# Optimization experiments

Measured on AMD Instinct MI355X. Metric: run time of the kernel, lower is better.

The kernel has to match this reference:

```python
import jax, jax.numpy as jnp
import numpy as np

B, N, DIM = 8, 8192, 256
K, CDIM = 4096, 1024
COMMIT = 0.25


def setup_inputs() -> dict:
    key = jax.random.key(0)
    ks = jax.random.split(key, 4)
    x = jax.random.normal(ks[0], (B, N, DIM), dtype=jnp.float32)
    ln_g = jnp.ones((DIM,), jnp.float32)
    ln_b = jnp.zeros((DIM,), jnp.float32)
    w_pre = jax.random.normal(ks[1], (DIM, CDIM), jnp.float32) / np.sqrt(DIM)
    b_pre = jnp.zeros((CDIM,), jnp.float32)
    embed = jax.random.normal(ks[2], (K, CDIM), jnp.float32)
    w_post = jax.random.normal(ks[3], (CDIM, DIM), jnp.float32) / np.sqrt(CDIM)
    b_post = jnp.zeros((DIM,), jnp.float32)
    return {"x": x, "ln_g": ln_g, "ln_b": ln_b, "w_pre": w_pre, "b_pre": b_pre,
            "embed": embed, "w_post": w_post, "b_post": b_post}


def reference(x, ln_g, ln_b, w_pre, b_pre, embed, w_post, b_post):
    # LayerNorm over last dim (eps=1e-5, torch default)
    mu = jnp.mean(x, axis=-1, keepdims=True)
    var = jnp.mean((x - mu) ** 2, axis=-1, keepdims=True)
    xn = (x - mu) * jax.lax.rsqrt(var + 1e-5) * ln_g + ln_b
    # GELU (exact, erf-based as in torch default) then Linear dim->codebook_dim
    z_e = jax.nn.gelu(xn, approximate=False) @ w_pre + b_pre  # (B,N,CDIM)
    flat = z_e.reshape(-1, CDIM)                              # (B*N, CDIM)
    # squared euclidean distances to codebook, argmin, gather
    z_sq = jnp.sum(flat * flat, axis=1, keepdims=True)        # (BN,1)
    e_sq = jnp.sum(embed * embed, axis=1)                     # (K,)
    dist = z_sq - 2.0 * (flat @ embed.T) + e_sq[None, :]      # (BN,K)
    indices = jnp.argmin(dist, axis=1)                        # (BN,)
    z_q = embed[indices]                                      # (BN,CDIM)
    # commitment loss (z_q detached)
    commit = COMMIT * jnp.mean((flat - jax.lax.stop_gradient(z_q)) ** 2)
    # straight-through estimator
    z_q_st = flat + jax.lax.stop_gradient(z_q - flat)
    z_q_st = z_q_st.reshape(B, N, CDIM)
    quantized = z_q_st @ w_post + b_post                      # (B,N,DIM)
    return quantized, indices.reshape(B, N), commit
```

## Files before the change

### kernel.cpp

```cpp
#include <hip/hip_runtime.h>

#define BN_ROWS 65536
#define DIMX 256
#define CDIM 1024
#define KCODES 4096
#define NSP 16
#define CMARG 2.5f
#define RMARG 1.2f
#define FLT_BIG 3.402823466e+38f

static const size_t OFF_ESQ   = 0;
static const size_t OFF_IDXF  = 16384;
static const size_t OFF_CROW  = 278528;
static const size_t OFF_EPOST = 540672;
static const size_t OFF_EH    = 4734976;
static const size_t OFF_NFLAG = 13123584;
static const size_t OFF_FLAG  = 13123648;
static const size_t OFF_CAND  = 13385792;

typedef __attribute__((ext_vector_type(8))) short bf16x8;
typedef __attribute__((ext_vector_type(4))) float f32x4;

#define GLOAD_LDS16(gsrc, ldst)                                                \
  __builtin_amdgcn_global_load_lds(                                            \
      (const __attribute__((address_space(1))) void*)(gsrc),                   \
      (__attribute__((address_space(3))) void*)(ldst), 16, 0, 0)

template <int VMC>
__device__ __forceinline__ void wait_vm() {
  if constexpr (VMC == 8)
    asm volatile("s_waitcnt vmcnt(8)" ::: "memory");
  else if constexpr (VMC == 4)
    asm volatile("s_waitcnt vmcnt(4)" ::: "memory");
  else
    asm volatile("s_waitcnt vmcnt(0)" ::: "memory");
}

__device__ inline unsigned short bf_rtn(float f) {
  unsigned u = __float_as_uint(f);
  unsigned r = (u + 0x7FFFu + ((u >> 16) & 1u)) >> 16;
  return (unsigned short)r;
}
__device__ inline unsigned fkey(float s) {
  unsigned b = __float_as_uint(s);
  return b ^ ((unsigned)((int)b >> 31) | 0x80000000u);
}
__device__ inline float keyinv(unsigned k) {
  unsigned b = (k & 0x80000000u) ? (k ^ 0x80000000u) : ~k;
  return __uint_as_float(b);
}

__global__ __launch_bounds__(256) void k_esq(const float* __restrict__ embed,
                                             float* __restrict__ e_sq) {
  const int t = threadIdx.x, wv = t >> 6, lane = t & 63;
  const int row = blockIdx.x * 4 + wv;
  const float* e = embed + (size_t)row * CDIM;
  float s = 0.f;
  for (int k = lane * 4; k < CDIM; k += 256) {
    float4 v = *(const float4*)(e + k);
    s = fmaf(v.x, v.x, s); s = fmaf(v.y, v.y, s);
    s = fmaf(v.z, v.z, s); s = fmaf(v.w, v.w, s);
  }
#pragma unroll
  for (int o = 32; o > 0; o >>= 1) s += __shfl_xor(s, o);
  if (lane == 0) e_sq[row] = s;
}

__global__ __launch_bounds__(256) void k_ehi(const float* __restrict__ embed,
                                             short* __restrict__ Eh) {
  const int t = threadIdx.x;
  const size_t row = blockIdx.x;
  float4 v = *(const float4*)(embed + row * CDIM + t * 4);
  *(short4*)(Eh + row * CDIM + t * 4) =
      make_short4((short)bf_rtn(v.x), (short)bf_rtn(v.y), (short)bf_rtn(v.z),
                  (short)bf_rtn(v.w));
}

__global__ __launch_bounds__(256) void k_ln_gelu_gemm(
    const float* __restrict__ x, const float* __restrict__ ln_g,
    const float* __restrict__ ln_b, const float* __restrict__ w_pre,
    const float* __restrict__ b_pre, float* __restrict__ zf,
    short* __restrict__ zh, int row0) {
  __shared__ float g[16][DIMX];
  const int t = threadIdx.x;
  const int lrow0 = blockIdx.x * 16;
  const int grow0 = row0 + lrow0;
  const int wv = t >> 6, lane = t & 63;
#pragma unroll
  for (int j = 0; j < 4; ++j) {
    const int r = wv * 4 + j;
    const float* xr = x + (size_t)(grow0 + r) * DIMX;
    float4 v = *(const float4*)(xr + lane * 4);
    float s = v.x + v.y + v.z + v.w;
    float ss = v.x * v.x + v.y * v.y + v.z * v.z + v.w * v.w;
#pragma unroll
    for (int o = 32; o > 0; o >>= 1) { s += __shfl_xor(s, o); ss += __shfl_xor(ss, o); }
    const float mu = s * (1.0f / 256.0f);
    const float var = ss * (1.0f / 256.0f) - mu * mu;
    const float rstd = rsqrtf(var + 1e-5f);
    float vv[4] = {v.x, v.y, v.z, v.w};
#pragma unroll
    for (int q = 0; q < 4; ++q) {
      const int d = lane * 4 + q;
      float xn = (vv[q] - mu) * rstd * ln_g[d] + ln_b[d];
      g[r][d] = 0.5f * xn * (1.0f + erff(xn * 0.70710678118654752f));
    }
  }
  __syncthreads();
  float acc[16][4];
#pragma unroll
  for (int r = 0; r < 16; ++r)
#pragma unroll
    for (int c = 0; c < 4; ++c) acc[r][c] = 0.f;
#pragma unroll 4
  for (int d = 0; d < DIMX; ++d) {
    float4 w = *(const float4*)(w_pre + (size_t)d * CDIM + t * 4);
#pragma unroll
    for (int r = 0; r < 16; ++r) {
      const float gv = g[r][d];
      acc[r][0] = fmaf(gv, w.x, acc[r][0]);
      acc[r][1] = fmaf(gv, w.y, acc[r][1]);
      acc[r][2] = fmaf(gv, w.z, acc[r][2]);
      acc[r][3] = fmaf(gv, w.w, acc[r][3]);
    }
  }
  float4 bp = *(const float4*)(b_pre + t * 4);
#pragma unroll
  for (int r = 0; r < 16; ++r) {
    float4 o;
    o.x = acc[r][0] + bp.x; o.y = acc[r][1] + bp.y;
    o.z = acc[r][2] + bp.z; o.w = acc[r][3] + bp.w;
    *(float4*)(zf + (size_t)(lrow0 + r) * CDIM + t * 4) = o;
    *(short4*)(zh + (size_t)(lrow0 + r) * CDIM + t * 4) =
        make_short4((short)bf_rtn(o.x), (short)bf_rtn(o.y), (short)bf_rtn(o.z),
                    (short)bf_rtn(o.w));
  }
}

__global__ __launch_bounds__(512) void k_score(
    const short* __restrict__ Eh, const short* __restrict__ Zh,
    const float* __restrict__ e_sq, uint2* __restrict__ cand, int chunk) {
  __shared__ __align__(16) short lds[4][16384];
  const int t = threadIdx.x;
  const int cpx = gridDim.x >> 3;
  const int bx = (blockIdx.x & 7) * cpx + (blockIdx.x >> 3);
  const int zblk = bx / NSP, csp = bx % NSP;
  const int wid = t >> 6, l = t & 63;
  const int wr = wid >> 2, wc = wid & 3;
  const int lg = l >> 4, lo16 = l & 15;
  const int rowbase = zblk * 256;
  const int m0 = csp * 256;
  const int wr8 = wr * 8, wc4 = wc * 4, l8 = l * 8;

  const bool isA = (wid < 4);
  const int q = wid & 3;
  const short* sarr = isA ? Eh : Zh;
  const int sbase = isA ? m0 : rowbase;
  const short* sp0 = sarr + (size_t)(sbase + q * 64 + lo16) * 1024 + lg * 8;
  const int dstbase = (isA ? 0 : 8192) + q * 4 * 512;

  f32x4 acc[8][4];
#pragma unroll
  for (int mi = 0; mi < 8; ++mi)
#pragma unroll
    for (int ni = 0; ni < 4; ++ni) acc[mi][ni] = (f32x4){0.f, 0.f, 0.f, 0.f};

#pragma unroll
  for (int pk = 0; pk < 3; ++pk) {
    const short* sp = sp0 + pk * 32;
    short* D = &lds[pk][dstbase];
#pragma unroll
    for (int u = 0; u < 4; ++u) GLOAD_LDS16(sp + u * 16384, D + u * 512);
  }

#define SCORE_KT(KT, VMC, ST)                                                  \
  {                                                                            \
    const short* Lc = lds[(KT) & 3];                                           \
    wait_vm<VMC>();                                                            \
    __builtin_amdgcn_s_barrier();                                              \
    __builtin_amdgcn_sched_barrier(0);                                         \
    bf16x8 bh[4], a[8];                                                        \
    _Pragma("unroll") for (int ni = 0; ni < 4; ++ni) bh[ni] =                  \
        *(const bf16x8*)(Lc + 8192 + (wc4 + ni) * 512 + l8);                   \
    _Pragma("unroll") for (int u = 0; u < 8; ++u) a[u] =                       \
        *(const bf16x8*)(Lc + (wr8 + u) * 512 + l8);                           \
    if (ST) {                                                                  \
      short* Dst = &lds[((KT) + 3) & 3][dstbase];                              \
      const short* spk = sp0 + ((KT) + 3) * 32;                                \
      _Pragma("unroll") for (int u = 0; u < 4; ++u)                            \
          GLOAD_LDS16(spk + u * 16384, Dst + u * 512);                         \
    }                                                                          \
    asm volatile("s_waitcnt lgkmcnt(0)" ::: "memory");                         \
    __builtin_amdgcn_sched_barrier(0);                                         \
    __builtin_amdgcn_s_setprio(1);                                             \
    _Pragma("unroll") for (int u = 0; u < 8; ++u)                              \
        _Pragma("unroll") for (int ni = 0; ni < 4; ++ni) acc[u][ni] =          \
            __builtin_amdgcn_mfma_f32_16x16x32_bf16(a[u], bh[ni],              \
                                                    acc[u][ni], 0, 0, 0);      \
    __builtin_amdgcn_s_setprio(0);                                             \
  }

  for (int kt = 0; kt < 30; ++kt) SCORE_KT(kt, 8, (kt < 29));
  SCORE_KT(30, 4, false);
  SCORE_KT(31, 0, false);
#undef SCORE_KT

  float s1[4];
  int i1[4];
#pragma unroll
  for (int i = 0; i < 4; ++i) { s1[i] = FLT_BIG; i1[i] = 0x7fffffff; }
#pragma unroll
  for (int mi = 0; mi < 8; ++mi) {
    const int c0 = m0 + wr * 128 + mi * 16 + lg * 4;
    float4 es = *(const float4*)(e_sq + c0);
    float esv[4] = {es.x, es.y, es.z, es.w};
#pragma unroll
    for (int ni = 0; ni < 4; ++ni) {
#pragma unroll
      for (int j = 0; j < 4; ++j) {
        const float s = fmaf(-2.0f, acc[mi][ni][j], esv[j]);
        const int c = c0 + j;
        if (s < s1[ni] || (s == s1[ni] && c < i1[ni])) { s1[ni] = s; i1[ni] = c; }
      }
    }
  }

  unsigned long long* red = (unsigned long long*)&lds[0][0];
  float* sb = (float*)&lds[0][2048];
  unsigned* sbi = (unsigned*)&lds[0][2560];
  unsigned* cnt = (unsigned*)&lds[0][3072];
  uint2* slot = (uint2*)&lds[0][3584];

  __syncthreads();
#pragma unroll
  for (int ni = 0; ni < 4; ++ni) {
    unsigned long long k1v =
        (((unsigned long long)fkey(s1[ni])) << 32) | (unsigned)i1[ni];
    unsigned long long o1 = __shfl_xor(k1v, 16);
    k1v = o1 < k1v ? o1 : k1v;
    o1 = __shfl_xor(k1v, 32);
    k1v = o1 < k1v ? o1 : k1v;
    if (lg == 0) {
      const int r = wc * 64 + ni * 16 + lo16;
      red[r * 2 + wr] = k1v;
    }
  }
  __syncthreads();
  if (t < 256) {
    unsigned long long a1 = red[t * 2 + 0], b1 = red[t * 2 + 1];
    if (b1 < a1) a1 = b1;
    sb[t] = keyinv((unsigned)(a1 >> 32));
    sbi[t] = (unsigned)(a1 & 0xFFFFFFFFull);
    cnt[t] = 0;
  }
  __syncthreads();
#pragma unroll
  for (int mi = 0; mi < 8; ++mi) {
    const int c0 = m0 + wr * 128 + mi * 16 + lg * 4;
    float4 es = *(const float4*)(e_sq + c0);
    float esv[4] = {es.x, es.y, es.z, es.w};
#pragma unroll
    for (int ni = 0; ni < 4; ++ni) {
      const int r = wc * 64 + ni * 16 + lo16;
      const float thr = sb[r] + CMARG;
#pragma unroll
      for (int j = 0; j < 4; ++j) {
        const float s = fmaf(-2.0f, acc[mi][ni][j], esv[j]);
        const unsigned c = (unsigned)(c0 + j);
        if (s < thr && c != sbi[r]) {
          unsigned pos = atomicAdd(&cnt[r], 1u);
          if (pos < 3) slot[r * 3 + pos] = make_uint2(__float_as_uint(s), c);
        }
      }
    }
  }
  __syncthreads();
  if (t < 256) {
    uint2* g = cand + ((size_t)(rowbase + t) * NSP + csp) * 4;
    const unsigned ov = (cnt[t] > 3) ? 0x40000000u : 0u;
    g[0] = make_uint2(__float_as_uint(sb[t]), sbi[t] | ov);
    const unsigned n = cnt[t] > 3 ? 3 : cnt[t];
#pragma unroll
    for (int k = 0; k < 3; ++k)
      g[1 + k] = (k < (int)n) ? slot[t * 3 + k]
                              : make_uint2(__float_as_uint(FLT_BIG), 0xFFFFFFFFu);
  }
}

__global__ __launch_bounds__(256) void k_refine(
    const uint2* __restrict__ cand, const float* __restrict__ zf,
    const float* __restrict__ embed, int* __restrict__ idxf,
    float* __restrict__ crow, float* __restrict__ out_idx,
    int* __restrict__ flag_rows, int* __restrict__ nflag, int chunk,
    int row0) {
  const int t = threadIdx.x, wid = t >> 6, l = t & 63;
  const int lrow = blockIdx.x * 4 + wid;
  if (lrow >= chunk) return;
  const int grow = row0 + lrow;
  const uint2 cs = cand[(size_t)lrow * 64 + l];
  const float sc = __uint_as_float(cs.x);
  const unsigned raw = cs.y;
  const bool isMin = (l & 3) == 0;
  float gm = isMin ? sc : FLT_BIG;
#pragma unroll
  for (int o = 32; o > 0; o >>= 1) gm = fminf(gm, __shfl_xor(gm, o));
  const float thr = gm + RMARG;
  const bool ovf = __any(isMin && (raw & 0x40000000u) && (sc < thr));

  float zv[16];
#pragma unroll
  for (int j = 0; j < 16; ++j) zv[j] = zf[(size_t)lrow * CDIM + l + 64 * j];

  const int myidx = (int)(raw & 0xFFFFu);
  const bool valid = (sc < thr) && (myidx < KCODES);
  unsigned long long mask = __ballot(valid);
  double d1 = 1e300;
  int i1 = 0x7fffffff;
  while (mask) {
    const int src = __ffsll((unsigned long long)mask) - 1;
    mask &= mask - 1;
    const int c = __shfl(myidx, src);
    const float* e = embed + (size_t)c * CDIM;
    double dd = 0.0;
#pragma unroll
    for (int j = 0; j < 16; ++j) {
      const double df = (double)zv[j] - (double)e[l + 64 * j];
      dd = fma(df, df, dd);
    }
#pragma unroll
    for (int o = 32; o > 0; o >>= 1) dd += __shfl_xor(dd, o);
    if (dd < d1 || (dd == d1 && c < i1)) { d1 = dd; i1 = c; }
  }
  if (l == 0) {
    idxf[grow] = i1;
    out_idx[grow] = (float)i1;
    crow[grow] = (float)d1;
    if (ovf) {
      const int s = atomicAdd(nflag, 1);
      flag_rows[s] = lrow;
    }
  }
}

__global__ __launch_bounds__(256) void k_exact(
    const float* __restrict__ zf, const float* __restrict__ embed,
    const int* __restrict__ flag_rows, const int* __restrict__ nflag,
    int* __restrict__ idxf, float* __restrict__ crow,
    float* __restrict__ out_idx, int row0) {
  __shared__ double wd[4];
  __shared__ int wcidx[4];
  const int t = threadIdx.x;
  const int wid = t >> 6, l = t & 63;
  const int n = *nflag;

  for (int fi = blockIdx.x; fi < n; fi += gridDim.x) {
    const int lrow = flag_rows[fi];
    const int grow = row0 + lrow;
    float zr[16];
#pragma unroll
    for (int j = 0; j < 16; ++j) zr[j] = zf[(size_t)lrow * CDIM + l + 64 * j];
    double dmin = 1e300;
    int cmin = 0x7fffffff;
    for (int ci = 0; ci < 1024; ++ci) {
      const int c = wid * 1024 + ci;
      const float* e = embed + (size_t)c * CDIM;
      double dd = 0.0;
#pragma unroll
      for (int j = 0; j < 16; ++j) {
        const double df = (double)zr[j] - (double)e[l + 64 * j];
        dd = fma(df, df, dd);
      }
#pragma unroll
      for (int o = 32; o > 0; o >>= 1) dd += __shfl_xor(dd, o);
      if (dd < dmin) { dmin = dd; cmin = c; }
    }
    if (l == 0) { wd[wid] = dmin; wcidx[wid] = cmin; }
    __syncthreads();
    if (t == 0) {
      double dm = wd[0]; int cm = wcidx[0];
#pragma unroll
      for (int wv = 1; wv < 4; ++wv) {
        if (wd[wv] < dm || (wd[wv] == dm && wcidx[wv] < cm)) {
          dm = wd[wv]; cm = wcidx[wv];
        }
      }
      idxf[grow] = cm;
      out_idx[grow] = (float)cm;
      crow[grow] = (float)dm;
    }
    __syncthreads();
  }
}

__global__ __launch_bounds__(256) void k_epost(const float* __restrict__ E,
                                               const float* __restrict__ w_post,
                                               float* __restrict__ E_post) {
  __shared__ float es[16][128];
  const int t = threadIdx.x;
  const int r0 = blockIdx.x * 16;
  float acc[16];
#pragma unroll
  for (int r = 0; r < 16; ++r) acc[r] = 0.f;
  for (int k0 = 0; k0 < CDIM; k0 += 128) {
    __syncthreads();
#pragma unroll
    for (int p = 0; p < 2; ++p) {
      const int fl = (p * 256 + t) * 4;
      const int r = fl >> 7, kk = fl & 127;
      float4 v = *(const float4*)(E + (size_t)(r0 + r) * CDIM + k0 + kk);
      *(float4*)&es[r][kk] = v;
    }
    __syncthreads();
#pragma unroll 4
    for (int d = 0; d < 128; ++d) {
      const float w = w_post[(size_t)(k0 + d) * DIMX + t];
#pragma unroll
      for (int r = 0; r < 16; ++r) acc[r] = fmaf(es[r][d], w, acc[r]);
    }
  }
#pragma unroll
  for (int r = 0; r < 16; ++r)
    E_post[(size_t)(r0 + r) * DIMX + t] = acc[r];
}

__global__ __launch_bounds__(256) void k_gather(const float* __restrict__ E_post,
                                                const int* __restrict__ idx,
                                                const float* __restrict__ b_post,
                                                float* __restrict__ outq) {
  const int t = threadIdx.x;
  const int r0 = blockIdx.x * 16;
  const float bp = b_post[t];
#pragma unroll
  for (int i = 0; i < 16; ++i) {
    const int row = r0 + i;
    outq[(size_t)row * DIMX + t] = E_post[(size_t)idx[row] * DIMX + t] + bp;
  }
}

__global__ __launch_bounds__(256) void k_commit_final(
    const float* __restrict__ crow, float* __restrict__ out_commit) {
  const int t = threadIdx.x;
  double s = 0.0;
  for (int i = t; i < BN_ROWS; i += 256) s += (double)crow[i];
#pragma unroll
  for (int o = 32; o > 0; o >>= 1) s += __shfl_xor(s, o);
  __shared__ double wsum[4];
  if ((t & 63) == 0) wsum[t >> 6] = s;
  __syncthreads();
  if (t == 0)
    *out_commit = (float)(0.25 * (wsum[0] + wsum[1] + wsum[2] + wsum[3]) /
                          (65536.0 * 1024.0));
}

extern "C" void kernel_launch(void* const* d_in, const int* in_sizes, int n_in,
                              void* d_out, int out_size, void* d_ws,
                              size_t ws_size, hipStream_t stream) {
  const float* x = (const float*)d_in[0];
  const float* ln_g = (const float*)d_in[1];
  const float* ln_b = (const float*)d_in[2];
  const float* w_pre = (const float*)d_in[3];
  const float* b_pre = (const float*)d_in[4];
  const float* embed = (const float*)d_in[5];
  const float* w_post = (const float*)d_in[6];
  const float* b_post = (const float*)d_in[7];

  float* out = (float*)d_out;
  float* outq = out;
  float* out_idx = out + 16777216;
  float* out_commit = out + 16842752;

  char* ws = (char*)d_ws;
  float* e_sq = (float*)(ws + OFF_ESQ);
  int* idxf = (int*)(ws + OFF_IDXF);
  float* crow = (float*)(ws + OFF_CROW);
  float* E_post = (float*)(ws + OFF_EPOST);
  short* Eh = (short*)(ws + OFF_EH);
  int* nflag = (int*)(ws + OFF_NFLAG);
  int* flag_rows = (int*)(ws + OFF_FLAG);

  int chunk = 4096;
  while (chunk < BN_ROWS &&
         OFF_CAND + (size_t)(chunk * 2) * 6656ull <= ws_size)
    chunk *= 2;
  uint2* cand = (uint2*)(ws + OFF_CAND);
  short* zh = (short*)(ws + OFF_CAND + (size_t)chunk * 512);
  float* zf = (float*)(ws + OFF_CAND + (size_t)chunk * 512 + (size_t)chunk * 2048);

  k_esq<<<KCODES / 4, 256, 0, stream>>>(embed, e_sq);
  k_ehi<<<KCODES, 256, 0, stream>>>(embed, Eh);
  k_epost<<<KCODES / 16, 256, 0, stream>>>(embed, w_post, E_post);

  for (int row0 = 0; row0 < BN_ROWS; row0 += chunk) {
    hipMemsetAsync(nflag, 0, sizeof(int), stream);
    k_ln_gelu_gemm<<<chunk / 16, 256, 0, stream>>>(x, ln_g, ln_b, w_pre, b_pre,
                                                   zf, zh, row0);
    k_score<<<(chunk / 256) * NSP, 512, 0, stream>>>(Eh, zh, e_sq, cand, chunk);
    k_refine<<<chunk / 4, 256, 0, stream>>>(cand, zf, embed, idxf, crow,
                                            out_idx, flag_rows, nflag, chunk,
                                            row0);
    k_exact<<<128, 256, 0, stream>>>(zf, embed, flag_rows, nflag, idxf, crow,
                                     out_idx, row0);
  }

  k_gather<<<BN_ROWS / 16, 256, 0, stream>>>(E_post, idxf, b_post, outq);
  k_commit_final<<<1, 256, 0, stream>>>(crow, out_commit);
}
```

Measured before the change: 1.456 ms.

## Switch codebook scoring GEMM from bf16 to int8 MFMA with wider candidate margins

Quantizes the codebook and z_e to int8 with a fixed scale and runs the distance-scoring GEMM with i32 16x16x64 int8 MFMA instead of bf16. This halves operand bytes and K-loop iterations in the score kernel. Because int8 is coarser, the candidate margin and slot count per split grow (11 slots, margins of 24), so the refine kernel checks more candidates in fp64. The trade is more refine work and wider candidate storage, plus overflow-flag fallbacks if the fixed scale clips values.

```diff
diff --git a/kernel.cpp b/kernel.cpp
--- a/kernel.cpp
+++ b/kernel.cpp
@@ -5,21 +5,24 @@
 #define CDIM 1024
 #define KCODES 4096
 #define NSP 16
-#define CMARG 2.5f
-#define RMARG 1.2f
+#define NSLOT 11
+#define NENT 12
+#define CMARG 24.0f
+#define RMARG 24.0f
+#define QS 24.0f
+#define INV_S2 (1.0f / (QS * QS))
 #define FLT_BIG 3.402823466e+38f
 
 static const size_t OFF_ESQ   = 0;
 static const size_t OFF_IDXF  = 16384;
 static const size_t OFF_CROW  = 278528;
 static const size_t OFF_EPOST = 540672;
-static const size_t OFF_EH    = 4734976;
-static const size_t OFF_NFLAG = 13123584;
-static const size_t OFF_FLAG  = 13123648;
-static const size_t OFF_CAND  = 13385792;
-
-typedef __attribute__((ext_vector_type(8))) short bf16x8;
-typedef __attribute__((ext_vector_type(4))) float f32x4;
+static const size_t OFF_EI8   = 4734976;
+static const size_t OFF_NFLAG = 8929280;
+static const size_t OFF_FLAG  = 8929344;
+static const size_t OFF_CAND  = 9191488;
+
+typedef __attribute__((ext_vector_type(4))) int i32x4;
 
 #define GLOAD_LDS16(gsrc, ldst)                                                \
   __builtin_amdgcn_global_load_lds(                                            \
@@ -36,10 +39,8 @@
     asm volatile("s_waitcnt vmcnt(0)" ::: "memory");
 }
 
-__device__ inline unsigned short bf_rtn(float f) {
-  unsigned u = __float_as_uint(f);
-  unsigned r = (u + 0x7FFFu + ((u >> 16) & 1u)) >> 16;
-  return (unsigned short)r;
+__device__ inline char q8(float f) {
+  return (char)__float2int_rn(fminf(fmaxf(f * QS, -127.f), 127.f));
 }
 __device__ inline unsigned fkey(float s) {
   unsigned b = __float_as_uint(s);
@@ -66,21 +67,20 @@
   if (lane == 0) e_sq[row] = s;
 }
 
-__global__ __launch_bounds__(256) void k_ehi(const float* __restrict__ embed,
-                                             short* __restrict__ Eh) {
+__global__ __launch_bounds__(256) void k_ei8(const float* __restrict__ embed,
+                                             char* __restrict__ Ei8) {
   const int t = threadIdx.x;
   const size_t row = blockIdx.x;
   float4 v = *(const float4*)(embed + row * CDIM + t * 4);
-  *(short4*)(Eh + row * CDIM + t * 4) =
-      make_short4((short)bf_rtn(v.x), (short)bf_rtn(v.y), (short)bf_rtn(v.z),
-                  (short)bf_rtn(v.w));
+  *(char4*)(Ei8 + row * CDIM + t * 4) =
+      make_char4(q8(v.x), q8(v.y), q8(v.z), q8(v.w));
 }
 
 __global__ __launch_bounds__(256) void k_ln_gelu_gemm(
     const float* __restrict__ x, const float* __restrict__ ln_g,
     const float* __restrict__ ln_b, const float* __restrict__ w_pre,
     const float* __restrict__ b_pre, float* __restrict__ zf,
-    short* __restrict__ zh, int row0) {
+    char* __restrict__ zi8, int row0) {
   __shared__ float g[16][DIMX];
   const int t = threadIdx.x;
   const int lrow0 = blockIdx.x * 16;
@@ -131,16 +131,15 @@
     o.x = acc[r][0] + bp.x; o.y = acc[r][1] + bp.y;
     o.z = acc[r][2] + bp.z; o.w = acc[r][3] + bp.w;
     *(float4*)(zf + (size_t)(lrow0 + r) * CDIM + t * 4) = o;
-    *(short4*)(zh + (size_t)(lrow0 + r) * CDIM + t * 4) =
-        make_short4((short)bf_rtn(o.x), (short)bf_rtn(o.y), (short)bf_rtn(o.z),
-                    (short)bf_rtn(o.w));
+    *(char4*)(zi8 + (size_t)(lrow0 + r) * CDIM + t * 4) =
+        make_char4(q8(o.x), q8(o.y), q8(o.z), q8(o.w));
   }
 }
 
 __global__ __launch_bounds__(512) void k_score(
-    const short* __restrict__ Eh, const short* __restrict__ Zh,
+    const char* __restrict__ Ei8, const char* __restrict__ Zi8,
     const float* __restrict__ e_sq, uint2* __restrict__ cand, int chunk) {
-  __shared__ __align__(16) short lds[4][16384];
+  __shared__ __align__(16) char lds[4][32768];
   const int t = threadIdx.x;
   const int cpx = gridDim.x >> 3;
   const int bx = (blockIdx.x & 7) * cpx + (blockIdx.x >> 3);
@@ -150,59 +149,59 @@
   const int lg = l >> 4, lo16 = l & 15;
   const int rowbase = zblk * 256;
   const int m0 = csp * 256;
-  const int wr8 = wr * 8, wc4 = wc * 4, l8 = l * 8;
+  const int wr8 = wr * 8, wc4 = wc * 4, l16 = l * 16;
 
   const bool isA = (wid < 4);
   const int q = wid & 3;
-  const short* sarr = isA ? Eh : Zh;
+  const char* sarr = isA ? Ei8 : Zi8;
   const int sbase = isA ? m0 : rowbase;
-  const short* sp0 = sarr + (size_t)(sbase + q * 64 + lo16) * 1024 + lg * 8;
-  const int dstbase = (isA ? 0 : 8192) + q * 4 * 512;
-
-  f32x4 acc[8][4];
+  const char* sp0 = sarr + (size_t)(sbase + q * 64 + lo16) * 1024 + lg * 16;
+  const int dstbase = (isA ? 0 : 16384) + q * 4096;
+
+  i32x4 acc[8][4];
 #pragma unroll
   for (int mi = 0; mi < 8; ++mi)
 #pragma unroll
-    for (int ni = 0; ni < 4; ++ni) acc[mi][ni] = (f32x4){0.f, 0.f, 0.f, 0.f};
+    for (int ni = 0; ni < 4; ++ni) acc[mi][ni] = (i32x4){0, 0, 0, 0};
 
 #pragma unroll
   for (int pk = 0; pk < 3; ++pk) {
-    const short* sp = sp0 + pk * 32;
-    short* D = &lds[pk][dstbase];
-#pragma unroll
-    for (int u = 0; u < 4; ++u) GLOAD_LDS16(sp + u * 16384, D + u * 512);
+    const char* sp = sp0 + pk * 64;
+    char* D = &lds[pk][dstbase];
+#pragma unroll
+    for (int u = 0; u < 4; ++u) GLOAD_LDS16(sp + u * 16384, D + u * 1024);
   }
 
 #define SCORE_KT(KT, VMC, ST)                                                  \
   {                                                                            \
-    const short* Lc = lds[(KT) & 3];                                           \
+    const char* Lc = lds[(KT) & 3];                                            \
     wait_vm<VMC>();                                                            \
     __builtin_amdgcn_s_barrier();                                              \
     __builtin_amdgcn_sched_barrier(0);                                         \
-    bf16x8 bh[4], a[8];                                                        \
+    i32x4 bh[4], a[8];                                                         \
     _Pragma("unroll") for (int ni = 0; ni < 4; ++ni) bh[ni] =                  \
-        *(const bf16x8*)(Lc + 8192 + (wc4 + ni) * 512 + l8);                   \
+        *(const i32x4*)(Lc + 16384 + (wc4 + ni) * 1024 + l16);                 \
     _Pragma("unroll") for (int u = 0; u < 8; ++u) a[u] =                       \
-        *(const bf16x8*)(Lc + (wr8 + u) * 512 + l8);                           \
+        *(const i32x4*)(Lc + (wr8 + u) * 1024 + l16);                          \
     if (ST) {                                                                  \
-      short* Dst = &lds[((KT) + 3) & 3][dstbase];                              \
-      const short* spk = sp0 + ((KT) + 3) * 32;                                \
+      char* Dst = &lds[((KT) + 3) & 3][dstbase];                               \
+      const char* spk = sp0 + ((KT) + 3) * 64;                                 \
       _Pragma("unroll") for (int u = 0; u < 4; ++u)                            \
-          GLOAD_LDS16(spk + u * 16384, Dst + u * 512);                         \
+          GLOAD_LDS16(spk + u * 16384, Dst + u * 1024);                        \
     }                                                                          \
     asm volatile("s_waitcnt lgkmcnt(0)" ::: "memory");                         \
     __builtin_amdgcn_sched_barrier(0);                                         \
     __builtin_amdgcn_s_setprio(1);                                             \
     _Pragma("unroll") for (int u = 0; u < 8; ++u)                              \
         _Pragma("unroll") for (int ni = 0; ni < 4; ++ni) acc[u][ni] =          \
-            __builtin_amdgcn_mfma_f32_16x16x32_bf16(a[u], bh[ni],              \
-                                                    acc[u][ni], 0, 0, 0);      \
+            __builtin_amdgcn_mfma_i32_16x16x64_i8(a[u], bh[ni],                \
+                                                  acc[u][ni], 0, 0, 0);        \
     __builtin_amdgcn_s_setprio(0);                                             \
   }
 
-  for (int kt = 0; kt < 30; ++kt) SCORE_KT(kt, 8, (kt < 29));
-  SCORE_KT(30, 4, false);
-  SCORE_KT(31, 0, false);
+  for (int kt = 0; kt < 14; ++kt) SCORE_KT(kt, 8, (kt < 13));
+  SCORE_KT(14, 4, false);
+  SCORE_KT(15, 0, false);
 #undef SCORE_KT
 
   float s1[4];
@@ -218,7 +217,7 @@
     for (int ni = 0; ni < 4; ++ni) {
 #pragma unroll
       for (int j = 0; j < 4; ++j) {
-        const float s = fmaf(-2.0f, acc[mi][ni][j], esv[j]);
+        const float s = fmaf(-2.0f * INV_S2, (float)acc[mi][ni][j], esv[j]);
         const int c = c0 + j;
         if (s < s1[ni] || (s == s1[ni] && c < i1[ni])) { s1[ni] = s; i1[ni] = c; }
       }
@@ -226,10 +225,10 @@
   }
 
   unsigned long long* red = (unsigned long long*)&lds[0][0];
-  float* sb = (float*)&lds[0][2048];
-  unsigned* sbi = (unsigned*)&lds[0][2560];
-  unsigned* cnt = (unsigned*)&lds[0][3072];
-  uint2* slot = (uint2*)&lds[0][3584];
+  float* sb = (float*)&lds[0][4096];
+  unsigned* sbi = (unsigned*)&lds[0][5120];
+  unsigned* cnt = (unsigned*)&lds[0][6144];
+  uint2* slot = (uint2*)&lds[0][7168];
 
   __syncthreads();
 #pragma unroll
@@ -265,24 +264,25 @@
       const float thr = sb[r] + CMARG;
 #pragma unroll
       for (int j = 0; j < 4; ++j) {
-        const float s = fmaf(-2.0f, acc[mi][ni][j], esv[j]);
+        const float s = fmaf(-2.0f * INV_S2, (float)acc[mi][ni][j], esv[j]);
         const unsigned c = (unsigned)(c0 + j);
         if (s < thr && c != sbi[r]) {
           unsigned pos = atomicAdd(&cnt[r], 1u);
-          if (pos < 3) slot[r * 3 + pos] = make_uint2(__float_as_uint(s), c);
+          if (pos < NSLOT)
+            slot[r * NSLOT + pos] = make_uint2(__float_as_uint(s), c);
         }
       }
     }
   }
   __syncthreads();
   if (t < 256) {
-    uint2* g = cand + ((size_t)(rowbase + t) * NSP + csp) * 4;
-    const unsigned ov = (cnt[t] > 3) ? 0x40000000u : 0u;
+    uint2* g = cand + (size_t)(rowbase + t) * (NSP * NENT) + csp * NENT;
+    const unsigned ov = (cnt[t] > NSLOT) ? 0x40000000u : 0u;
     g[0] = make_uint2(__float_as_uint(sb[t]), sbi[t] | ov);
-    const unsigned n = cnt[t] > 3 ? 3 : cnt[t];
-#pragma unroll
-    for (int k = 0; k < 3; ++k)
-      g[1 + k] = (k < (int)n) ? slot[t * 3 + k]
+    const unsigned n = cnt[t] > NSLOT ? NSLOT : cnt[t];
+#pragma unroll
+    for (int k = 0; k < NSLOT; ++k)
+      g[1 + k] = (k < (int)n) ? slot[t * NSLOT + k]
                               : make_uint2(__float_as_uint(FLT_BIG), 0xFFFFFFFFu);
   }
 }
@@ -297,40 +297,55 @@
   const int lrow = blockIdx.x * 4 + wid;
   if (lrow >= chunk) return;
   const int grow = row0 + lrow;
-  const uint2 cs = cand[(size_t)lrow * 64 + l];
-  const float sc = __uint_as_float(cs.x);
-  const unsigned raw = cs.y;
-  const bool isMin = (l & 3) == 0;
-  float gm = isMin ? sc : FLT_BIG;
+  const uint2* base = cand + (size_t)lrow * (NSP * NENT);
+  const uint2 e0 = base[l];
+  const uint2 e1 = base[64 + l];
+  const uint2 e2 = base[128 + l];
+  const bool is0 = (l % NENT) == 0;
+  const bool is1 = ((l + 64) % NENT) == 0;
+  const bool is2 = ((l + 128) % NENT) == 0;
+  float gm = FLT_BIG;
+  if (is0) gm = fminf(gm, __uint_as_float(e0.x));
+  if (is1) gm = fminf(gm, __uint_as_float(e1.x));
+  if (is2) gm = fminf(gm, __uint_as_float(e2.x));
 #pragma unroll
   for (int o = 32; o > 0; o >>= 1) gm = fminf(gm, __shfl_xor(gm, o));
   const float thr = gm + RMARG;
-  const bool ovf = __any(isMin && (raw & 0x40000000u) && (sc < thr));
+  bool myovf = (is0 && (e0.y & 0x40000000u) && __uint_as_float(e0.x) < thr) ||
+               (is1 && (e1.y & 0x40000000u) && __uint_as_float(e1.x) < thr) ||
+               (is2 && (e2.y & 0x40000000u) && __uint_as_float(e2.x) < thr);
+  const bool ovf = __any(myovf);
 
   float zv[16];
 #pragma unroll
   for (int j = 0; j < 16; ++j) zv[j] = zf[(size_t)lrow * CDIM + l + 64 * j];
 
-  const int myidx = (int)(raw & 0xFFFFu);
-  const bool valid = (sc < thr) && (myidx < KCODES);
-  unsigned long long mask = __ballot(valid);
   double d1 = 1e300;
   int i1 = 0x7fffffff;
-  while (mask) {
-    const int src = __ffsll((unsigned long long)mask) - 1;
-    mask &= mask - 1;
-    const int c = __shfl(myidx, src);
-    const float* e = embed + (size_t)c * CDIM;
-    double dd = 0.0;
-#pragma unroll
-    for (int j = 0; j < 16; ++j) {
-      const double df = (double)zv[j] - (double)e[l + 64 * j];
-      dd = fma(df, df, dd);
-    }
-#pragma unroll
-    for (int o = 32; o > 0; o >>= 1) dd += __shfl_xor(dd, o);
-    if (dd < d1 || (dd == d1 && c < i1)) { d1 = dd; i1 = c; }
-  }
+#define PROC(E)                                                                \
+  {                                                                            \
+    const float sc_ = __uint_as_float(E.x);                                    \
+    const int id_ = (int)(E.y & 0xFFFFu);                                      \
+    unsigned long long mask = __ballot(sc_ < thr && id_ < KCODES);             \
+    while (mask) {                                                             \
+      const int src = __ffsll((unsigned long long)mask) - 1;                   \
+      mask &= mask - 1;                                                        \
+      const int c = __shfl(id_, src);                                          \
+      const float* e = embed + (size_t)c * CDIM;                               \
+      double dd = 0.0;                                                         \
+      _Pragma("unroll") for (int j = 0; j < 16; ++j) {                         \
+        const double df = (double)zv[j] - (double)e[l + 64 * j];               \
+        dd = fma(df, df, dd);                                                  \
+      }                                                                        \
+      _Pragma("unroll") for (int o = 32; o > 0; o >>= 1) dd +=                 \
+          __shfl_xor(dd, o);                                                   \
+      if (dd < d1 || (dd == d1 && c < i1)) { d1 = dd; i1 = c; }                \
+    }                                                                          \
+  }
+  PROC(e0);
+  PROC(e1);
+  PROC(e2);
+#undef PROC
   if (l == 0) {
     idxf[grow] = i1;
     out_idx[grow] = (float)i1;
@@ -474,7 +489,7 @@
   int* idxf = (int*)(ws + OFF_IDXF);
   float* crow = (float*)(ws + OFF_CROW);
   float* E_post = (float*)(ws + OFF_EPOST);
-  short* Eh = (short*)(ws + OFF_EH);
+  char* Ei8 = (char*)(ws + OFF_EI8);
   int* nflag = (int*)(ws + OFF_NFLAG);
   int* flag_rows = (int*)(ws + OFF_FLAG);
 
@@ -483,18 +498,20 @@
          OFF_CAND + (size_t)(chunk * 2) * 6656ull <= ws_size)
     chunk *= 2;
   uint2* cand = (uint2*)(ws + OFF_CAND);
-  short* zh = (short*)(ws + OFF_CAND + (size_t)chunk * 512);
-  float* zf = (float*)(ws + OFF_CAND + (size_t)chunk * 512 + (size_t)chunk * 2048);
+  char* zi8 = ws + OFF_CAND + (size_t)chunk * 1536;
+  float* zf = (float*)(ws + OFF_CAND + (size_t)chunk * 1536 +
+                       (size_t)chunk * 1024);
 
   k_esq<<<KCODES / 4, 256, 0, stream>>>(embed, e_sq);
-  k_ehi<<<KCODES, 256, 0, stream>>>(embed, Eh);
+  k_ei8<<<KCODES, 256, 0, stream>>>(embed, Ei8);
   k_epost<<<KCODES / 16, 256, 0, stream>>>(embed, w_post, E_post);
 
   for (int row0 = 0; row0 < BN_ROWS; row0 += chunk) {
     hipMemsetAsync(nflag, 0, sizeof(int), stream);
     k_ln_gelu_gemm<<<chunk / 16, 256, 0, stream>>>(x, ln_g, ln_b, w_pre, b_pre,
-                                                   zf, zh, row0);
-    k_score<<<(chunk / 256) * NSP, 512, 0, stream>>>(Eh, zh, e_sq, cand, chunk);
+                                                   zf, zi8, row0);
+    k_score<<<(chunk / 256) * NSP, 512, 0, stream>>>(Ei8, zi8, e_sq, cand,
+                                                     chunk);
     k_refine<<<chunk / 4, 256, 0, stream>>>(cand, zf, embed, idxf, crow,
                                             out_idx, flag_rows, nflag, chunk,
                                             row0);
```

Measured after the change: 1.364 ms. 6.3% less time.
